# Performance work log

Hardware: AMD Instinct MI355X
Metric: run time of the kernel (lower is better)

## Reference

```python
import jax, jax.numpy as jnp
import numpy as np

N_NODES = 50000
N_EDGES = 800000
D = 128
BN_EPS = 1e-5


def gcn_conv(x, src, dst, W, b, n_nodes):
    # x: [N, Din]; src/dst: [E+N] (self-loops already appended)
    h = x @ W  # [N, Dout]
    deg = jax.ops.segment_sum(jnp.ones_like(src, dtype=h.dtype), dst, num_segments=n_nodes)
    dinv = jnp.where(deg > 0, jax.lax.rsqrt(deg), 0.0)  # deg^{-1/2}
    norm = dinv[src] * dinv[dst]  # [E+N]
    msg = h[src] * norm[:, None]  # gather + scale
    out = jax.ops.segment_sum(msg, dst, num_segments=n_nodes)  # scatter-add
    return out + b


def batchnorm_prelu(x, gamma, beta, a):
    # training-mode BN over node dim (biased variance), then PReLU
    mu = jnp.mean(x, axis=0)
    var = jnp.mean(jnp.square(x - mu), axis=0)
    xn = (x - mu) * jax.lax.rsqrt(var + BN_EPS)
    y = xn * gamma + beta
    return jnp.where(y >= 0, y, a * y)


def setup_inputs():
    key = jax.random.key(0)
    ks = jax.random.split(key, 8)
    x = jax.random.normal(ks[0], (N_NODES, D), dtype=jnp.float32)
    edge_index = jax.random.randint(ks[1], (2, N_EDGES), 0, N_NODES, dtype=jnp.int32)
    lim = float(np.sqrt(6.0 / (D + D)))  # glorot
    W1 = jax.random.uniform(ks[2], (D, D), jnp.float32, -lim, lim)
    W2 = jax.random.uniform(ks[3], (D, D), jnp.float32, -lim, lim)
    b1 = jnp.zeros((D,), jnp.float32)
    b2 = jnp.zeros((D,), jnp.float32)
    gamma1 = jnp.ones((D,), jnp.float32)
    beta1 = jnp.zeros((D,), jnp.float32)
    gamma2 = jnp.ones((D,), jnp.float32)
    beta2 = jnp.zeros((D,), jnp.float32)
    a1 = jnp.full((1,), 0.25, jnp.float32)
    a2 = jnp.full((1,), 0.25, jnp.float32)
    return {"x": x, "edge_index": edge_index, "W1": W1, "b1": b1, "gamma1": gamma1,
            "beta1": beta1, "a1": a1, "W2": W2, "b2": b2, "gamma2": gamma2,
            "beta2": beta2, "a2": a2}


def reference(x, edge_index, W1, b1, gamma1, beta1, a1, W2, b2, gamma2, beta2, a2):
    n = x.shape[0]
    loops = jnp.arange(n, dtype=edge_index.dtype)
    src = jnp.concatenate([edge_index[0], loops])
    dst = jnp.concatenate([edge_index[1], loops])
    h = gcn_conv(x, src, dst, W1, b1, n)
    h = batchnorm_prelu(h, gamma1, beta1, a1)
    h = gcn_conv(h, src, dst, W2, b2, n)
    h = batchnorm_prelu(h, gamma2, beta2, a2)
    return h
```

## Files before the change

### kernel.cpp

```cpp
#include <hip/hip_runtime.h>
#include <hip/hip_bf16.h>

#define N_NODES 50000
#define N_EDGES 800000
#define D 128
#define BN_EPS 1e-5f
#define GEMM_ROWS 128
#define LDS_PITCH 136

#define BSH 8
#define NB 196
#define TILE 4096
#define NTILES ((N_EDGES + TILE - 1) / TILE)
#define REC_CAP 6144

typedef unsigned short u16;
typedef short bf16x8 __attribute__((ext_vector_type(8)));
typedef float f32x4  __attribute__((ext_vector_type(4)));

__device__ __forceinline__ u16 f2bf(float f) {
    union { float f; unsigned int u; } v; v.f = f;
    unsigned int u = v.u;
    return (u16)((u + 0x7FFF + ((u >> 16) & 1)) >> 16);
}
__device__ __forceinline__ float bflo(unsigned int u) {
    union { unsigned int u; float f; } v; v.u = u << 16; return v.f;
}
__device__ __forceinline__ float bfhi(unsigned int u) {
    union { unsigned int u; float f; } v; v.u = u & 0xFFFF0000u; return v.f;
}
__device__ __forceinline__ unsigned int packbf(float a, float b) {
    return (unsigned int)f2bf(a) | ((unsigned int)f2bf(b) << 16);
}

__global__ __launch_bounds__(256) void bucket_hist(const int* __restrict__ dst,
                                                   int* __restrict__ btot) {
    __shared__ int h[256];
    const int t  = threadIdx.x;
    const int e0 = blockIdx.x * TILE;
    h[t] = 0;
    __syncthreads();
#pragma unroll
    for (int i = 0; i < 16; ++i) {
        int e = e0 + t + 256 * i;
        if (e < N_EDGES) atomicAdd(&h[dst[e] >> BSH], 1);
    }
    __syncthreads();
    if (t < NB && h[t] > 0) atomicAdd(&btot[t], h[t]);
}

__global__ __launch_bounds__(256) void bucket_scan(const int* __restrict__ btot,
                                                   int* __restrict__ bbase,
                                                   int* __restrict__ bcur,
                                                   int* __restrict__ row_ptr) {
    __shared__ int s[256];
    const int t = threadIdx.x;
    int v = (t < NB) ? btot[t] : 0;
    s[t] = v;
    __syncthreads();
#pragma unroll
    for (int off = 1; off < 256; off <<= 1) {
        int add = (t >= off) ? s[t - off] : 0;
        __syncthreads();
        s[t] += add;
        __syncthreads();
    }
    if (t < NB) { bbase[t] = s[t] - v; bcur[t] = s[t] - v; }
    if (t == 0) row_ptr[N_NODES] = N_EDGES;
}

__global__ __launch_bounds__(256) void bucket_scatter(const int* __restrict__ src,
                                                      const int* __restrict__ dst,
                                                      int* __restrict__ bcur,
                                                      unsigned int* __restrict__ brec) {
    __shared__ int h[256];
    __shared__ int sb[256];
    __shared__ int lbase[256];
    __shared__ int lcur[256];
    __shared__ int gbase[256];
    __shared__ unsigned int  rec[TILE];
    __shared__ unsigned char rbk[TILE];
    const int t  = threadIdx.x;
    const int e0 = blockIdx.x * TILE;
    const int tcount = min(TILE, N_EDGES - e0);

    h[t] = 0;
    __syncthreads();

    unsigned int myrec[16];
    int          myb[16];
#pragma unroll
    for (int i = 0; i < 16; ++i) {
        int e = e0 + t + 256 * i;
        if (e < N_EDGES) {
            unsigned int s_ = (unsigned int)src[e];
            unsigned int d_ = (unsigned int)dst[e];
            int b = (int)(d_ >> BSH);
            myb[i]   = b;
            myrec[i] = s_ | ((d_ & 255u) << 16);
            atomicAdd(&h[b], 1);
        } else myb[i] = -1;
    }
    __syncthreads();
    sb[t] = h[t];
    __syncthreads();
#pragma unroll
    for (int off = 1; off < 256; off <<= 1) {
        int add = (t >= off) ? sb[t - off] : 0;
        __syncthreads();
        sb[t] += add;
        __syncthreads();
    }
    lbase[t] = sb[t] - h[t];
    lcur[t]  = sb[t] - h[t];
    __syncthreads();
#pragma unroll
    for (int i = 0; i < 16; ++i) {
        if (myb[i] >= 0) {
            int p = atomicAdd(&lcur[myb[i]], 1);
            rec[p] = myrec[i];
            rbk[p] = (unsigned char)myb[i];
        }
    }
    __syncthreads();
    if (t < NB && h[t] > 0) gbase[t] = atomicAdd(&bcur[t], h[t]);
    __syncthreads();
    for (int i = t; i < tcount; i += 256) {
        int b = rbk[i];
        brec[gbase[b] + (i - lbase[b])] = rec[i];
    }
}

__global__ __launch_bounds__(256) void bucket_csr(const unsigned int* __restrict__ brec,
                                                  const int* __restrict__ bbase,
                                                  const int* __restrict__ btot,
                                                  int* __restrict__ row_ptr,
                                                  u16* __restrict__ col,
                                                  float* __restrict__ dinv) {
    __shared__ unsigned int rec[REC_CAP];
    __shared__ u16 cls[REC_CAP];
    __shared__ int h[256];
    __shared__ int sb[256];
    __shared__ int lcur[256];
    const int b    = blockIdx.x;
    const int t    = threadIdx.x;
    const int base = bbase[b];
    const int cnt  = min(btot[b], REC_CAP);
    const int n0   = b << BSH;
    const int nn   = min(256, N_NODES - n0);

    for (int i = t; i < cnt; i += 256) rec[i] = brec[base + i];
    h[t] = 0;
    __syncthreads();
    for (int i = t; i < cnt; i += 256) atomicAdd(&h[(rec[i] >> 16) & 255u], 1);
    __syncthreads();
    sb[t] = h[t];
    __syncthreads();
#pragma unroll
    for (int off = 1; off < 256; off <<= 1) {
        int add = (t >= off) ? sb[t - off] : 0;
        __syncthreads();
        sb[t] += add;
        __syncthreads();
    }
    int excl = sb[t] - h[t];
    lcur[t] = excl;
    if (t < nn) {
        row_ptr[n0 + t] = base + excl;
        dinv[n0 + t]    = rsqrtf((float)h[t] + 1.0f);
    }
    __syncthreads();
    for (int i = t; i < cnt; i += 256) {
        unsigned int r = rec[i];
        int p = atomicAdd(&lcur[(r >> 16) & 255u], 1);
        cls[p] = (u16)(r & 0xFFFFu);
    }
    __syncthreads();
    for (int i = t; i < cnt; i += 256) col[base + i] = cls[i];
}

__global__ __launch_bounds__(256) void w_prep(const float* __restrict__ W1,
                                              const float* __restrict__ W2,
                                              u16* __restrict__ Wt1,
                                              u16* __restrict__ Wt2) {
    int t = blockIdx.x * blockDim.x + threadIdx.x;
    const float* W = (t < 16384) ? W1 : W2;
    u16* Wt        = (t < 16384) ? Wt1 : Wt2;
    int u = t & 16383;
    int k = u >> 7, n = u & 127;
    Wt[n * 128 + k] = f2bf(W[u]);
}

template <bool BN_IN>
__global__ __launch_bounds__(256) void gemm_bf16(const void* __restrict__ Xv,
                                                 const u16* __restrict__ Wt,
                                                 u16* __restrict__ C,
                                                 const float* __restrict__ dinv,
                                                 const float* __restrict__ sums,
                                                 const float* __restrict__ gamma,
                                                 const float* __restrict__ beta,
                                                 const float* __restrict__ a,
                                                 int nrows) {
    __shared__ u16 As[GEMM_ROWS * LDS_PITCH];
    __shared__ u16 Ws[128 * LDS_PITCH];
    const int tid  = threadIdx.x;
    const int row0 = blockIdx.x * GEMM_ROWS;
    const float invN = 1.0f / (float)N_NODES;

    const bf16x8* Wt8 = (const bf16x8*)Wt;
#pragma unroll
    for (int i = 0; i < 8; ++i) {
        int u = tid + 256 * i;
        int n = u >> 4, kg = u & 15;
        *(bf16x8*)&Ws[n * LDS_PITCH + kg * 8] = Wt8[u];
    }

    if (BN_IN) {
        const uint4* X4 = (const uint4*)Xv;
        const float av = a[0];
#pragma unroll
        for (int i = 0; i < 8; ++i) {
            int u    = tid + 256 * i;
            int r    = u >> 4, kg = u & 15;
            int grow = row0 + r;
            uint4 o = make_uint4(0, 0, 0, 0);
            if (grow < nrows) {
                uint4 v = X4[(size_t)grow * 16 + kg];
                float f[8] = { bflo(v.x), bfhi(v.x), bflo(v.y), bfhi(v.y),
                               bflo(v.z), bfhi(v.z), bflo(v.w), bfhi(v.w) };
#pragma unroll
                for (int c = 0; c < 8; ++c) {
                    int fe     = kg * 8 + c;
                    float mean = sums[fe] * invN;
                    float var  = sums[128 + fe] * invN - mean * mean;
                    float sc   = rsqrtf(var + BN_EPS) * gamma[fe];
                    float y    = (f[c] - mean) * sc + beta[fe];
                    f[c]       = (y >= 0.f) ? y : av * y;
                }
                o.x = packbf(f[0], f[1]); o.y = packbf(f[2], f[3]);
                o.z = packbf(f[4], f[5]); o.w = packbf(f[6], f[7]);
            }
            *(uint4*)&As[r * LDS_PITCH + kg * 8] = o;
        }
    } else {
        const float4* X4 = (const float4*)Xv;
#pragma unroll
        for (int i = 0; i < 16; ++i) {
            int u    = tid + 256 * i;
            int r    = u >> 5, kf = u & 31;
            int grow = row0 + r;
            float4 v = make_float4(0.f, 0.f, 0.f, 0.f);
            if (grow < nrows) v = X4[(size_t)grow * 32 + kf];
            ushort4 p;
            p.x = f2bf(v.x); p.y = f2bf(v.y); p.z = f2bf(v.z); p.w = f2bf(v.w);
            *(ushort4*)&As[r * LDS_PITCH + kf * 4] = p;
        }
    }
    __syncthreads();

    const int wv   = tid >> 6;
    const int lane = tid & 63;
    const int n    = lane & 15;
    const int q    = lane >> 4;
    const int c0   = wv * 32;

    bf16x8 bfr[4][2];
#pragma unroll
    for (int kb = 0; kb < 4; ++kb)
#pragma unroll
        for (int c = 0; c < 2; ++c)
            bfr[kb][c] = *(const bf16x8*)&Ws[(c0 + 16 * c + n) * LDS_PITCH + 32 * kb + 8 * q];

    f32x4 acc[8][2];
    const f32x4 z = {0.f, 0.f, 0.f, 0.f};
#pragma unroll
    for (int rt = 0; rt < 8; ++rt) { acc[rt][0] = z; acc[rt][1] = z; }

#pragma unroll
    for (int kb = 0; kb < 4; ++kb) {
#pragma unroll
        for (int rt = 0; rt < 8; ++rt) {
            bf16x8 af = *(const bf16x8*)&As[(16 * rt + n) * LDS_PITCH + 32 * kb + 8 * q];
            acc[rt][0] = __builtin_amdgcn_mfma_f32_16x16x32_bf16(af, bfr[kb][0], acc[rt][0], 0, 0, 0);
            acc[rt][1] = __builtin_amdgcn_mfma_f32_16x16x32_bf16(af, bfr[kb][1], acc[rt][1], 0, 0, 0);
        }
    }

#pragma unroll
    for (int rt = 0; rt < 8; ++rt) {
        int gr0 = row0 + 16 * rt + 4 * q;
#pragma unroll
        for (int r = 0; r < 4; ++r) {
            int gr = gr0 + r;
            if (gr < nrows) {
                float dv = dinv[gr];
                C[(size_t)gr * D + c0 + n]      = f2bf(acc[rt][0][r] * dv);
                C[(size_t)gr * D + c0 + 16 + n] = f2bf(acc[rt][1][r] * dv);
            }
        }
    }
}

__global__ __launch_bounds__(256) void pull_agg(const u16* __restrict__ H,
                                                const int* __restrict__ row_ptr,
                                                const u16* __restrict__ col,
                                                const float* __restrict__ dinv,
                                                u16* __restrict__ out) {
    const int sub  = threadIdx.x & 15;
    const int grp  = (blockIdx.x * blockDim.x + threadIdx.x) >> 4;
    const int ngrp = (gridDim.x * blockDim.x) >> 4;
    const uint4* H4   = (const uint4*)H;
    uint4*       out4 = (uint4*)out;

    for (int d = grp; d < N_NODES; d += ngrp) {
        const int beg = row_ptr[d];
        const int end = row_ptr[d + 1];
        float a0[8], a1[8] = {}, a2[8] = {}, a3[8] = {};
        {
            uint4 v = H4[(size_t)d * 16 + sub];
            a0[0] = bflo(v.x); a0[1] = bfhi(v.x); a0[2] = bflo(v.y); a0[3] = bfhi(v.y);
            a0[4] = bflo(v.z); a0[5] = bfhi(v.z); a0[6] = bflo(v.w); a0[7] = bfhi(v.w);
        }
        int j = beg;
        for (; j + 3 < end; j += 4) {
            const int s0 = col[j], s1 = col[j + 1], s2 = col[j + 2], s3 = col[j + 3];
            const uint4 v0 = H4[(size_t)s0 * 16 + sub];
            const uint4 v1 = H4[(size_t)s1 * 16 + sub];
            const uint4 v2 = H4[(size_t)s2 * 16 + sub];
            const uint4 v3 = H4[(size_t)s3 * 16 + sub];
            a0[0] += bflo(v0.x); a0[1] += bfhi(v0.x); a0[2] += bflo(v0.y); a0[3] += bfhi(v0.y);
            a0[4] += bflo(v0.z); a0[5] += bfhi(v0.z); a0[6] += bflo(v0.w); a0[7] += bfhi(v0.w);
            a1[0] += bflo(v1.x); a1[1] += bfhi(v1.x); a1[2] += bflo(v1.y); a1[3] += bfhi(v1.y);
            a1[4] += bflo(v1.z); a1[5] += bfhi(v1.z); a1[6] += bflo(v1.w); a1[7] += bfhi(v1.w);
            a2[0] += bflo(v2.x); a2[1] += bfhi(v2.x); a2[2] += bflo(v2.y); a2[3] += bfhi(v2.y);
            a2[4] += bflo(v2.z); a2[5] += bfhi(v2.z); a2[6] += bflo(v2.w); a2[7] += bfhi(v2.w);
            a3[0] += bflo(v3.x); a3[1] += bfhi(v3.x); a3[2] += bflo(v3.y); a3[3] += bfhi(v3.y);
            a3[4] += bflo(v3.z); a3[5] += bfhi(v3.z); a3[6] += bflo(v3.w); a3[7] += bfhi(v3.w);
        }
        for (; j < end; ++j) {
            const uint4 v = H4[(size_t)col[j] * 16 + sub];
            a0[0] += bflo(v.x); a0[1] += bfhi(v.x); a0[2] += bflo(v.y); a0[3] += bfhi(v.y);
            a0[4] += bflo(v.z); a0[5] += bfhi(v.z); a0[6] += bflo(v.w); a0[7] += bfhi(v.w);
        }
        const float dv = dinv[d];
        float r[8];
#pragma unroll
        for (int c = 0; c < 8; ++c) r[c] = ((a0[c] + a1[c]) + (a2[c] + a3[c])) * dv;
        uint4 o;
        o.x = packbf(r[0], r[1]); o.y = packbf(r[2], r[3]);
        o.z = packbf(r[4], r[5]); o.w = packbf(r[6], r[7]);
        out4[(size_t)d * 16 + sub] = o;
    }
}

__global__ __launch_bounds__(256) void bn_reduce_bf(const u16* __restrict__ X,
                                                    float* __restrict__ sums, int n) {
    __shared__ float red[256];
    const int fp  = threadIdx.x & 63;
    const int rof = threadIdx.x >> 6;
    const unsigned int* X2 = (const unsigned int*)X;
    float s0 = 0.f, q0 = 0.f, s1 = 0.f, q1 = 0.f;
    for (int r = blockIdx.x * 4 + rof; r < n; r += gridDim.x * 4) {
        unsigned int u = X2[(size_t)r * 64 + fp];
        float v0 = bflo(u), v1 = bfhi(u);
        s0 += v0; q0 += v0 * v0; s1 += v1; q1 += v1 * v1;
    }
    red[threadIdx.x] = s0; __syncthreads();
    if (rof == 0) s0 = red[fp] + red[fp + 64] + red[fp + 128] + red[fp + 192];
    __syncthreads(); red[threadIdx.x] = q0; __syncthreads();
    if (rof == 0) q0 = red[fp] + red[fp + 64] + red[fp + 128] + red[fp + 192];
    __syncthreads(); red[threadIdx.x] = s1; __syncthreads();
    if (rof == 0) s1 = red[fp] + red[fp + 64] + red[fp + 128] + red[fp + 192];
    __syncthreads(); red[threadIdx.x] = q1; __syncthreads();
    if (rof == 0) {
        q1 = red[fp] + red[fp + 64] + red[fp + 128] + red[fp + 192];
        int f = fp * 2;
        atomicAdd(&sums[f], s0);       atomicAdd(&sums[128 + f], q0);
        atomicAdd(&sums[f + 1], s1);   atomicAdd(&sums[128 + f + 1], q1);
    }
}

__global__ void bn_prelu_bf(const u16* __restrict__ X, const float* __restrict__ sums,
                            const float* __restrict__ gamma, const float* __restrict__ beta,
                            const float* __restrict__ a, float* __restrict__ out,
                            float invN) {
    int idx = blockIdx.x * blockDim.x + threadIdx.x;
    if (idx >= N_NODES * 64) return;
    unsigned int u = ((const unsigned int*)X)[idx];
    int f0 = (idx * 2) & 127;
    float av = a[0];
    float2 o;
    {
        float mean = sums[f0] * invN;
        float var  = sums[128 + f0] * invN - mean * mean;
        float sc   = rsqrtf(var + BN_EPS) * gamma[f0];
        float y    = (bflo(u) - mean) * sc + beta[f0];
        o.x = (y >= 0.f) ? y : av * y;
    }
    {
        int f1 = f0 + 1;
        float mean = sums[f1] * invN;
        float var  = sums[128 + f1] * invN - mean * mean;
        float sc   = rsqrtf(var + BN_EPS) * gamma[f1];
        float y    = (bfhi(u) - mean) * sc + beta[f1];
        o.y = (y >= 0.f) ? y : av * y;
    }
    ((float2*)out)[idx] = o;
}

extern "C" void kernel_launch(void* const* d_in, const int* in_sizes, int n_in,
                              void* d_out, int out_size, void* d_ws, size_t ws_size,
                              hipStream_t stream) {
    const float* x      = (const float*)d_in[0];
    const int*   edges  = (const int*)d_in[1];
    const float* W1     = (const float*)d_in[2];
    const float* gamma1 = (const float*)d_in[4];
    const float* beta1  = (const float*)d_in[5];
    const float* a1     = (const float*)d_in[6];
    const float* W2     = (const float*)d_in[7];
    const float* gamma2 = (const float*)d_in[9];
    const float* beta2  = (const float*)d_in[10];
    const float* a2     = (const float*)d_in[11];

    const int* src = edges;
    const int* dst = edges + N_EDGES;

    float* OUT = (float*)d_out;
    char* ws = (char*)d_ws;
    u16*   Abf      = (u16*)ws;    ws += (size_t)N_NODES * D * sizeof(u16);
    u16*   Obf      = (u16*)ws;    ws += (size_t)N_NODES * D * sizeof(u16);
    float* dinv     = (float*)ws;  ws += N_NODES * sizeof(float);
    float* sums     = (float*)ws;  ws += 256 * sizeof(float);
    int*   row_ptr  = (int*)ws;    ws += (N_NODES + 1) * sizeof(int);
    int*   btot     = (int*)ws;    ws += NB * sizeof(int);
    int*   bbase    = (int*)ws;    ws += NB * sizeof(int);
    int*   bcur     = (int*)ws;    ws += NB * sizeof(int);
    unsigned int* brec = (unsigned int*)ws; ws += (size_t)N_EDGES * sizeof(unsigned int);
    u16*   col      = (u16*)ws;    ws += (size_t)N_EDGES * sizeof(u16);
    u16*   Wt1      = (u16*)ws;    ws += 16384 * sizeof(u16);
    u16*   Wt2      = (u16*)ws;    ws += 16384 * sizeof(u16);

    const float invN = 1.0f / (float)N_NODES;
    const int gemmGrid = (N_NODES + GEMM_ROWS - 1) / GEMM_ROWS;
    const int prGrid   = (N_NODES * 64 + 255) / 256;

    hipMemsetAsync(btot, 0, NB * sizeof(int), stream);
    bucket_hist<<<NTILES, 256, 0, stream>>>(dst, btot);
    bucket_scan<<<1, 256, 0, stream>>>(btot, bbase, bcur, row_ptr);
    bucket_scatter<<<NTILES, 256, 0, stream>>>(src, dst, bcur, brec);
    bucket_csr<<<NB, 256, 0, stream>>>(brec, bbase, btot, row_ptr, col, dinv);
    w_prep<<<128, 256, 0, stream>>>(W1, W2, Wt1, Wt2);

    gemm_bf16<false><<<gemmGrid, 256, 0, stream>>>(x, Wt1, Abf, dinv,
                                                   nullptr, nullptr, nullptr, nullptr, N_NODES);
    pull_agg<<<2048, 256, 0, stream>>>(Abf, row_ptr, col, dinv, Obf);
    hipMemsetAsync(sums, 0, 256 * sizeof(float), stream);
    bn_reduce_bf<<<512, 256, 0, stream>>>(Obf, sums, N_NODES);

    gemm_bf16<true><<<gemmGrid, 256, 0, stream>>>(Obf, Wt2, Abf, dinv,
                                                  sums, gamma1, beta1, a1, N_NODES);
    pull_agg<<<2048, 256, 0, stream>>>(Abf, row_ptr, col, dinv, Obf);
    hipMemsetAsync(sums, 0, 256 * sizeof(float), stream);
    bn_reduce_bf<<<512, 256, 0, stream>>>(Obf, sums, N_NODES);
    bn_prelu_bf<<<prGrid, 256, 0, stream>>>(Obf, sums, gamma2, beta2, a2, OUT, invN);
}
```

Measured before the change: 310.1 us.

## Fuse BN statistics into aggregation and merge histogram with weight prep

Folds the per-feature sum and sum-of-squares reduction into the pull aggregation kernel, so the separate reduction pass that re-read the aggregated output is gone. The bucket histogram now writes per-tile counts that the scan kernel sums, which removes the global atomics and a memset. Weight transpose and zeroing of the statistics buffer move into the histogram launch. This cuts several launches and memsets and one full read of the node features per layer. In exchange, the statistics are computed from fp32 values before bf16 rounding, and the scan serially sums about 196 tiles per thread.

Result: no change. 310.5 us (+0.1%).

```diff
diff --git a/kernel.cpp b/kernel.cpp
--- a/kernel.cpp
+++ b/kernel.cpp
@@ -33,29 +33,48 @@
     return (unsigned int)f2bf(a) | ((unsigned int)f2bf(b) << 16);
 }
 
-__global__ __launch_bounds__(256) void bucket_hist(const int* __restrict__ dst,
-                                                   int* __restrict__ btot) {
+__global__ __launch_bounds__(256) void hist_prep(const int* __restrict__ dst,
+                                                 const float* __restrict__ W1,
+                                                 const float* __restrict__ W2,
+                                                 int* __restrict__ thist,
+                                                 u16* __restrict__ Wt1,
+                                                 u16* __restrict__ Wt2,
+                                                 float* __restrict__ sums) {
     __shared__ int h[256];
-    const int t  = threadIdx.x;
-    const int e0 = blockIdx.x * TILE;
-    h[t] = 0;
-    __syncthreads();
-#pragma unroll
-    for (int i = 0; i < 16; ++i) {
-        int e = e0 + t + 256 * i;
-        if (e < N_EDGES) atomicAdd(&h[dst[e] >> BSH], 1);
-    }
-    __syncthreads();
-    if (t < NB && h[t] > 0) atomicAdd(&btot[t], h[t]);
-}
-
-__global__ __launch_bounds__(256) void bucket_scan(const int* __restrict__ btot,
+    const int t = threadIdx.x;
+    const int b = blockIdx.x;
+    if (b < NTILES) {
+        h[t] = 0;
+        __syncthreads();
+        const int e0 = b * TILE;
+#pragma unroll
+        for (int i = 0; i < 16; ++i) {
+            int e = e0 + t + 256 * i;
+            if (e < N_EDGES) atomicAdd(&h[dst[e] >> BSH], 1);
+        }
+        __syncthreads();
+        thist[b * 256 + t] = h[t];
+    } else {
+        const int wb = b - NTILES;
+        if (wb == 0) { sums[t] = 0.f; sums[256 + t] = 0.f; }
+        int u = wb * 256 + t;
+        const float* W = (u < 16384) ? W1 : W2;
+        u16* Wt        = (u < 16384) ? Wt1 : Wt2;
+        int v = u & 16383;
+        int k = v >> 7, n = v & 127;
+        Wt[n * 128 + k] = f2bf(W[v]);
+    }
+}
+
+__global__ __launch_bounds__(256) void bucket_scan(const int* __restrict__ thist,
+                                                   int* __restrict__ btot,
                                                    int* __restrict__ bbase,
                                                    int* __restrict__ bcur,
                                                    int* __restrict__ row_ptr) {
     __shared__ int s[256];
     const int t = threadIdx.x;
-    int v = (t < NB) ? btot[t] : 0;
+    int v = 0;
+    for (int i = 0; i < NTILES; ++i) v += thist[i * 256 + t];
     s[t] = v;
     __syncthreads();
 #pragma unroll
@@ -65,7 +84,7 @@
         s[t] += add;
         __syncthreads();
     }
-    if (t < NB) { bbase[t] = s[t] - v; bcur[t] = s[t] - v; }
+    if (t < NB) { btot[t] = v; bbase[t] = s[t] - v; bcur[t] = s[t] - v; }
     if (t == 0) row_ptr[N_NODES] = N_EDGES;
 }
 
@@ -179,18 +198,6 @@
     for (int i = t; i < cnt; i += 256) col[base + i] = cls[i];
 }
 
-__global__ __launch_bounds__(256) void w_prep(const float* __restrict__ W1,
-                                              const float* __restrict__ W2,
-                                              u16* __restrict__ Wt1,
-                                              u16* __restrict__ Wt2) {
-    int t = blockIdx.x * blockDim.x + threadIdx.x;
-    const float* W = (t < 16384) ? W1 : W2;
-    u16* Wt        = (t < 16384) ? Wt1 : Wt2;
-    int u = t & 16383;
-    int k = u >> 7, n = u & 127;
-    Wt[n * 128 + k] = f2bf(W[u]);
-}
-
 template <bool BN_IN>
 __global__ __launch_bounds__(256) void gemm_bf16(const void* __restrict__ Xv,
                                                  const u16* __restrict__ Wt,
@@ -301,16 +308,21 @@
     }
 }
 
-__global__ __launch_bounds__(256) void pull_agg(const u16* __restrict__ H,
-                                                const int* __restrict__ row_ptr,
-                                                const u16* __restrict__ col,
-                                                const float* __restrict__ dinv,
-                                                u16* __restrict__ out) {
+__global__ __launch_bounds__(256) void pull_agg_red(const u16* __restrict__ H,
+                                                    const int* __restrict__ row_ptr,
+                                                    const u16* __restrict__ col,
+                                                    const float* __restrict__ dinv,
+                                                    u16* __restrict__ out,
+                                                    float* __restrict__ sums) {
+    __shared__ float red[16 * 128];
     const int sub  = threadIdx.x & 15;
+    const int g    = threadIdx.x >> 4;
     const int grp  = (blockIdx.x * blockDim.x + threadIdx.x) >> 4;
     const int ngrp = (gridDim.x * blockDim.x) >> 4;
     const uint4* H4   = (const uint4*)H;
     uint4*       out4 = (uint4*)out;
+
+    float bs[8] = {}, bq[8] = {};
 
     for (int d = grp; d < N_NODES; d += ngrp) {
         const int beg = row_ptr[d];
@@ -345,38 +357,35 @@
         const float dv = dinv[d];
         float r[8];
 #pragma unroll
-        for (int c = 0; c < 8; ++c) r[c] = ((a0[c] + a1[c]) + (a2[c] + a3[c])) * dv;
+        for (int c = 0; c < 8; ++c) {
+            r[c] = ((a0[c] + a1[c]) + (a2[c] + a3[c])) * dv;
+            bs[c] += r[c];
+            bq[c] += r[c] * r[c];
+        }
         uint4 o;
         o.x = packbf(r[0], r[1]); o.y = packbf(r[2], r[3]);
         o.z = packbf(r[4], r[5]); o.w = packbf(r[6], r[7]);
         out4[(size_t)d * 16 + sub] = o;
     }
-}
-
-__global__ __launch_bounds__(256) void bn_reduce_bf(const u16* __restrict__ X,
-                                                    float* __restrict__ sums, int n) {
-    __shared__ float red[256];
-    const int fp  = threadIdx.x & 63;
-    const int rof = threadIdx.x >> 6;
-    const unsigned int* X2 = (const unsigned int*)X;
-    float s0 = 0.f, q0 = 0.f, s1 = 0.f, q1 = 0.f;
-    for (int r = blockIdx.x * 4 + rof; r < n; r += gridDim.x * 4) {
-        unsigned int u = X2[(size_t)r * 64 + fp];
-        float v0 = bflo(u), v1 = bfhi(u);
-        s0 += v0; q0 += v0 * v0; s1 += v1; q1 += v1 * v1;
-    }
-    red[threadIdx.x] = s0; __syncthreads();
-    if (rof == 0) s0 = red[fp] + red[fp + 64] + red[fp + 128] + red[fp + 192];
-    __syncthreads(); red[threadIdx.x] = q0; __syncthreads();
-    if (rof == 0) q0 = red[fp] + red[fp + 64] + red[fp + 128] + red[fp + 192];
-    __syncthreads(); red[threadIdx.x] = s1; __syncthreads();
-    if (rof == 0) s1 = red[fp] + red[fp + 64] + red[fp + 128] + red[fp + 192];
-    __syncthreads(); red[threadIdx.x] = q1; __syncthreads();
-    if (rof == 0) {
-        q1 = red[fp] + red[fp + 64] + red[fp + 128] + red[fp + 192];
-        int f = fp * 2;
-        atomicAdd(&sums[f], s0);       atomicAdd(&sums[128 + f], q0);
-        atomicAdd(&sums[f + 1], s1);   atomicAdd(&sums[128 + f + 1], q1);
+
+#pragma unroll
+    for (int c = 0; c < 8; ++c) red[g * 128 + sub * 8 + c] = bs[c];
+    __syncthreads();
+    if (threadIdx.x < 128) {
+        float acc = 0.f;
+#pragma unroll
+        for (int g2 = 0; g2 < 16; ++g2) acc += red[g2 * 128 + threadIdx.x];
+        atomicAdd(&sums[threadIdx.x], acc);
+    }
+    __syncthreads();
+#pragma unroll
+    for (int c = 0; c < 8; ++c) red[g * 128 + sub * 8 + c] = bq[c];
+    __syncthreads();
+    if (threadIdx.x < 128) {
+        float acc = 0.f;
+#pragma unroll
+        for (int g2 = 0; g2 < 16; ++g2) acc += red[g2 * 128 + threadIdx.x];
+        atomicAdd(&sums[128 + threadIdx.x], acc);
     }
 }
 
@@ -430,11 +439,12 @@
     u16*   Abf      = (u16*)ws;    ws += (size_t)N_NODES * D * sizeof(u16);
     u16*   Obf      = (u16*)ws;    ws += (size_t)N_NODES * D * sizeof(u16);
     float* dinv     = (float*)ws;  ws += N_NODES * sizeof(float);
-    float* sums     = (float*)ws;  ws += 256 * sizeof(float);
+    float* sums     = (float*)ws;  ws += 512 * sizeof(float);
     int*   row_ptr  = (int*)ws;    ws += (N_NODES + 1) * sizeof(int);
     int*   btot     = (int*)ws;    ws += NB * sizeof(int);
     int*   bbase    = (int*)ws;    ws += NB * sizeof(int);
     int*   bcur     = (int*)ws;    ws += NB * sizeof(int);
+    int*   thist    = (int*)ws;    ws += (size_t)NTILES * 256 * sizeof(int);
     unsigned int* brec = (unsigned int*)ws; ws += (size_t)N_EDGES * sizeof(unsigned int);
     u16*   col      = (u16*)ws;    ws += (size_t)N_EDGES * sizeof(u16);
     u16*   Wt1      = (u16*)ws;    ws += 16384 * sizeof(u16);
@@ -444,23 +454,17 @@
     const int gemmGrid = (N_NODES + GEMM_ROWS - 1) / GEMM_ROWS;
     const int prGrid   = (N_NODES * 64 + 255) / 256;
 
-    hipMemsetAsync(btot, 0, NB * sizeof(int), stream);
-    bucket_hist<<<NTILES, 256, 0, stream>>>(dst, btot);
-    bucket_scan<<<1, 256, 0, stream>>>(btot, bbase, bcur, row_ptr);
+    hist_prep<<<NTILES + 128, 256, 0, stream>>>(dst, W1, W2, thist, Wt1, Wt2, sums);
+    bucket_scan<<<1, 256, 0, stream>>>(thist, btot, bbase, bcur, row_ptr);
     bucket_scatter<<<NTILES, 256, 0, stream>>>(src, dst, bcur, brec);
     bucket_csr<<<NB, 256, 0, stream>>>(brec, bbase, btot, row_ptr, col, dinv);
-    w_prep<<<128, 256, 0, stream>>>(W1, W2, Wt1, Wt2);
 
     gemm_bf16<false><<<gemmGrid, 256, 0, stream>>>(x, Wt1, Abf, dinv,
                                                    nullptr, nullptr, nullptr, nullptr, N_NODES);
-    pull_agg<<<2048, 256, 0, stream>>>(Abf, row_ptr, col, dinv, Obf);
-    hipMemsetAsync(sums, 0, 256 * sizeof(float), stream);
-    bn_reduce_bf<<<512, 256, 0, stream>>>(Obf, sums, N_NODES);
+    pull_agg_red<<<2048, 256, 0, stream>>>(Abf, row_ptr, col, dinv, Obf, sums);
 
     gemm_bf16<true><<<gemmGrid, 256, 0, stream>>>(Obf, Wt2, Abf, dinv,
                                                   sums, gamma1, beta1, a1, N_NODES);
-    pull_agg<<<2048, 256, 0, stream>>>(Abf, row_ptr, col, dinv, Obf);
-    hipMemsetAsync(sums, 0, 256 * sizeof(float), stream);
-    bn_reduce_bf<<<512, 256, 0, stream>>>(Obf, sums, N_NODES);
-    bn_prelu_bf<<<prGrid, 256, 0, stream>>>(Obf, sums, gamma2, beta2, a2, OUT, invN);
-}
+    pull_agg_red<<<2048, 256, 0, stream>>>(Abf, row_ptr, col, dinv, Obf, sums + 256);
+    bn_prelu_bf<<<prGrid, 256, 0, stream>>>(Obf, sums + 256, gamma2, beta2, a2, OUT, invN);
+}
```
